# Kernel tuning notes

Measured on AMD Instinct MI355X. Metric: run time of the kernel, lower is better.

## Reference

```python
import jax, jax.numpy as jnp
import numpy as np

B, D, H, N, K, C = 1024, 256, 512, 100000, 96, 10


def setup_inputs() -> dict:
    key = jax.random.key(0)
    ks = jax.random.split(key, 16)
    s = 0.02
    return {
        "x": jax.random.normal(ks[0], (B, D), jnp.float32),
        "candidate_x": jax.random.normal(ks[1], (N, D), jnp.float32),
        "candidate_labels": jax.random.randint(ks[2], (N,), 0, C, jnp.int32),
        "W_enc": jax.random.normal(ks[3], (D, H), jnp.float32) * s,
        "b_enc": jnp.zeros((H,), jnp.float32),
        "W_key": jax.random.normal(ks[4], (H, H), jnp.float32) * s,
        "b_key": jnp.zeros((H,), jnp.float32),
        "W_val": jax.random.normal(ks[5], (H, H), jnp.float32) * s,
        "b_val": jnp.zeros((H,), jnp.float32),
        "E_label": jax.random.normal(ks[6], (C, H), jnp.float32) * s,
        "W_t1": jax.random.normal(ks[7], (H, H), jnp.float32) * s,
        "b_t1": jnp.zeros((H,), jnp.float32),
        "W_t2": jax.random.normal(ks[8], (H, H), jnp.float32) * s,
    }


def reference(x, candidate_x, candidate_labels, W_enc, b_enc, W_key, b_key,
              W_val, b_val, E_label, W_t1, b_t1, W_t2):
    # Encode queries and candidates
    x_enc = x @ W_enc + b_enc                       # [B, H]
    cand_enc = candidate_x @ W_enc + b_enc          # [N, H]
    x_key = x_enc @ W_key + b_key                   # [B, H]
    cand_keys = cand_enc @ W_key + b_key            # [N, H]

    # Negative euclidean distance via GEMM expansion (compute-efficient cdist)
    q2 = jnp.sum(x_key * x_key, axis=-1, keepdims=True)        # [B, 1]
    c2 = jnp.sum(cand_keys * cand_keys, axis=-1)               # [N]
    d2 = q2 + c2[None, :] - 2.0 * (x_key @ cand_keys.T)        # [B, N]
    sim = -jnp.sqrt(jnp.maximum(d2, 0.0))                      # [B, N]

    # Top-k retrieval
    top_sims, top_idx = jax.lax.top_k(sim, K)                  # [B, K]

    cand_vals = cand_enc @ W_val + b_val                       # [N, H]
    label_emb = E_label[candidate_labels]                      # [N, H]

    ctx_keys = cand_keys[top_idx]                              # [B, K, H]
    ctx_labels = label_emb[top_idx]                            # [B, K, H]
    _ = cand_vals[top_idx]  # gathered values (unused by the original math)

    # Attention over retrieved context (softmax of top-k similarities)
    attn = jax.nn.softmax(top_sims, axis=1)                    # [B, K]

    # Correction MLP T (dropout is identity in eval mode)
    diff = x_key[:, None, :] - ctx_keys                        # [B, K, H]
    t_out = jax.nn.relu(diff @ W_t1 + b_t1) @ W_t2             # [B, K, H]

    ctx_vec = jnp.sum(attn[..., None] * (ctx_labels + t_out), axis=1)  # [B, H]
    return x_enc + ctx_vec
```

## Files before the change

kernel.cpp:

```cpp
#include <hip/hip_runtime.h>
#include <cfloat>
#include <cmath>

#define B_ 1024
#define D_ 256
#define H_ 512
#define N_ 100000
#define K_ 96
#define C_ 10
#define SAMP 4096
#define CAPC 4096
#define RCAP 15

typedef __attribute__((ext_vector_type(8))) short bf16x8;
typedef __attribute__((ext_vector_type(4))) float f32x4;

__device__ __forceinline__ float bf2f(ushort h) {
    union { unsigned u; float f; } v; v.u = ((unsigned)h) << 16; return v.f;
}
__device__ __forceinline__ ushort f2bf(float f) {
    union { float f; unsigned u; } v; v.f = f;
    unsigned u = v.u;
    unsigned r = (u + 0x7fffu + ((u >> 16) & 1u)) >> 16;
    return (ushort)r;
}
__device__ __forceinline__ unsigned f2key(float f) {
    unsigned u = __float_as_uint(f);
    return (u & 0x80000000u) ? ~u : (u | 0x80000000u);
}
__device__ __forceinline__ float d2_of(float acc, float q2, float c2) {
    return fmaxf(fmaf(-2.f, acc, q2 + c2), 0.f);
}

#define GLDS(g, l)                                                            \
    __builtin_amdgcn_global_load_lds(                                         \
        (const __attribute__((address_space(1))) void*)(g),                   \
        (__attribute__((address_space(3))) void*)(l), 16, 0, 0)

#define FENCE() asm volatile("" ::: "memory")

template <int RELU>
__global__ __launch_bounds__(256) void gemm_nn(const float* __restrict__ A,
                                               const float* __restrict__ Bm,
                                               const float* __restrict__ bias,
                                               float* __restrict__ Cm,
                                               int M, int N, int Kd) {
    __shared__ float sA[16][68];
    __shared__ float sB[16][64];
    const int t  = threadIdx.x;
    const int tx = t & 15, ty = t >> 4;
    const int m0 = blockIdx.y * 64;
    const int n0 = blockIdx.x * 64;
    const int lr = t >> 2;
    const int lk = (t & 3) << 2;
    const int bk = t >> 4;
    const int bn = (t & 15) << 2;

    float acc[4][4] = {};
    for (int k0 = 0; k0 < Kd; k0 += 16) {
        float4 av = make_float4(0.f, 0.f, 0.f, 0.f);
        if (m0 + lr < M)
            av = *(const float4*)(A + (size_t)(m0 + lr) * Kd + k0 + lk);
        sA[lk + 0][lr] = av.x; sA[lk + 1][lr] = av.y;
        sA[lk + 2][lr] = av.z; sA[lk + 3][lr] = av.w;
        float4 bv = *(const float4*)(Bm + (size_t)(k0 + bk) * N + n0 + bn);
        *(float4*)&sB[bk][bn] = bv;
        __syncthreads();
#pragma unroll
        for (int kk = 0; kk < 16; ++kk) {
            float4 a4 = *(const float4*)&sA[kk][ty << 2];
            float4 b4 = *(const float4*)&sB[kk][tx << 2];
            float ar[4] = {a4.x, a4.y, a4.z, a4.w};
            float br[4] = {b4.x, b4.y, b4.z, b4.w};
#pragma unroll
            for (int i = 0; i < 4; ++i)
#pragma unroll
                for (int j = 0; j < 4; ++j)
                    acc[i][j] = fmaf(ar[i], br[j], acc[i][j]);
        }
        __syncthreads();
    }
#pragma unroll
    for (int i = 0; i < 4; ++i) {
        int row = m0 + (ty << 2) + i;
        if (row < M) {
            int col = n0 + (tx << 2);
            float b0 = 0.f, b1 = 0.f, b2 = 0.f, b3 = 0.f;
            if (bias) { b0 = bias[col]; b1 = bias[col + 1]; b2 = bias[col + 2]; b3 = bias[col + 3]; }
            float4 o;
            o.x = acc[i][0] + b0; o.y = acc[i][1] + b1;
            o.z = acc[i][2] + b2; o.w = acc[i][3] + b3;
            if (RELU) {
                o.x = fmaxf(o.x, 0.f); o.y = fmaxf(o.y, 0.f);
                o.z = fmaxf(o.z, 0.f); o.w = fmaxf(o.w, 0.f);
            }
            *(float4*)(Cm + (size_t)row * N + col) = o;
        }
    }
}

template <int MODE, int SWZ>
__global__ __launch_bounds__(256) void gemm_nt(const ushort* __restrict__ A,
                                               const ushort* __restrict__ Bv,
                                               const float* __restrict__ bias,
                                               const float* __restrict__ q2v,
                                               const float* __restrict__ c2v,
                                               const float* __restrict__ thrv,
                                               float* __restrict__ candV,
                                               int* __restrict__ candI,
                                               int* __restrict__ cnt,
                                               void* __restrict__ Cout,
                                               int M, int Nlim, int K,
                                               int ldc, int nvalid, int per) {
    int m0, n0;
    if (SWZ == 0) {
        m0 = blockIdx.y * 128; n0 = blockIdx.x * 128;
    } else if (SWZ == 1) {
        int bid = blockIdx.x;
        int xcd = bid & 7, slot = bid >> 3;
        m0 = (slot & 7) * 128;
        n0 = (xcd * per + (slot >> 3)) * 128;
        if (n0 >= nvalid || m0 >= M) return;
    } else {
        int bid = blockIdx.x;
        int xcd = bid & 7, slot = bid >> 3;
        n0 = (slot & 3) * 128;
        m0 = (xcd * per + (slot >> 2)) * 128;
        if (m0 >= M) return;
    }

    __shared__ __align__(16) char smem[32768];
    const int t = threadIdx.x;
    const int lane = t & 63, w = t >> 6;
    const int wm = w & 1, wn = w >> 1;

    f32x4 acc[4][4];
#pragma unroll
    for (int i = 0; i < 4; ++i)
#pragma unroll
        for (int j = 0; j < 4; ++j)
            acc[i][j] = (f32x4){0.f, 0.f, 0.f, 0.f};

    const int la = lane & 15, lk = lane >> 4;
    const int aoff = (wm * 64 + la) * 64 + lk * 16;
    const int boff = (wn * 64 + la) * 64 + lk * 16;
    const int r_ = t >> 2, cc_ = (t & 3);

    auto stage = [&](int k0, int buf) {
#pragma unroll
        for (int q = 0; q < 2; ++q) {
            int r = r_ + q * 64;
            int ar = m0 + r; ar = (ar < M) ? ar : (M - 1);
            GLDS(A + (size_t)ar * K + k0 + cc_ * 8,
                 (char*)smem + buf * 8192 + (q * 256 + t) * 16);
            int br = n0 + r; br = (br < Nlim) ? br : (Nlim - 1);
            GLDS(Bv + (size_t)br * K + k0 + cc_ * 8,
                 (char*)smem + 16384 + buf * 8192 + (q * 256 + t) * 16);
        }
    };

    stage(0, 0);
    int cur = 0;
    for (int k0 = 0; k0 < K; k0 += 32) {
        if (k0 + 32 < K) {
            stage(k0 + 32, cur ^ 1);
            FENCE();
            asm volatile("s_waitcnt vmcnt(4)" ::: "memory");
        } else {
            FENCE();
            asm volatile("s_waitcnt vmcnt(0)" ::: "memory");
        }
        __builtin_amdgcn_s_barrier(); FENCE();

        bf16x8 af[4], bfr[4];
        const char* pA = (const char*)smem + cur * 8192 + aoff;
        const char* pB = (const char*)smem + 16384 + cur * 8192 + boff;
#pragma unroll
        for (int i = 0; i < 4; ++i)
            af[i] = *(const bf16x8*)(pA + i * 1024);
#pragma unroll
        for (int j = 0; j < 4; ++j)
            bfr[j] = *(const bf16x8*)(pB + j * 1024);
#pragma unroll
        for (int i = 0; i < 4; ++i)
#pragma unroll
            for (int j = 0; j < 4; ++j)
                acc[i][j] = __builtin_amdgcn_mfma_f32_16x16x32_bf16(
                    af[i], bfr[j], acc[i][j], 0, 0, 0);

        FENCE();
        asm volatile("s_waitcnt lgkmcnt(0)" ::: "memory");
        __builtin_amdgcn_s_barrier(); FENCE();
        cur ^= 1;
    }

    const int rl = (lane >> 4) * 4, cl = lane & 15;

    if (MODE == 5) {
        float* stV = (float*)smem;
        int*   stI = (int*)(smem + 7680);
        int*   stC = (int*)(smem + 15360);
        for (int r = t; r < 128; r += 256) stC[r] = 0;
        __syncthreads();
#pragma unroll
        for (int i = 0; i < 4; ++i) {
#pragma unroll
            for (int v = 0; v < 4; ++v) {
                int rloc = wm * 64 + i * 16 + rl + v;
                int gr = m0 + rloc;
                float q2b = q2v[gr];
                float th = thrv[gr];
#pragma unroll
                for (int j = 0; j < 4; ++j) {
                    int gc = n0 + wn * 64 + j * 16 + cl;
                    if (gc < nvalid) {
                        float d2 = d2_of(acc[i][j][v], q2b, c2v[gc]);
                        if (d2 <= th) {
                            int p = atomicAdd(&stC[rloc], 1);
                            if (p < RCAP) {
                                stV[rloc * RCAP + p] = d2;
                                stI[rloc * RCAP + p] = gc;
                            } else {
                                int gp = atomicAdd(&cnt[gr], 1);
                                if (gp < CAPC) {
                                    candV[(size_t)gr * CAPC + gp] = d2;
                                    candI[(size_t)gr * CAPC + gp] = gc;
                                }
                            }
                        }
                    }
                }
            }
        }
        __syncthreads();
        for (int r = t; r < 128; r += 256) {
            int n = stC[r]; if (n > RCAP) n = RCAP;
            if (n > 0) {
                int gr = m0 + r;
                int gb = atomicAdd(&cnt[gr], n);
                for (int q = 0; q < n; ++q) {
                    int pos = gb + q;
                    if (pos < CAPC) {
                        candV[(size_t)gr * CAPC + pos] = stV[r * RCAP + q];
                        candI[(size_t)gr * CAPC + pos] = stI[r * RCAP + q];
                    }
                }
            }
        }
        return;
    }

#pragma unroll
    for (int i = 0; i < 4; ++i) {
#pragma unroll
        for (int j = 0; j < 4; ++j) {
            int gc = n0 + wn * 64 + j * 16 + cl;
#pragma unroll
            for (int v = 0; v < 4; ++v) {
                int gr = m0 + wm * 64 + i * 16 + rl + v;
                if (gr < M && gc < nvalid) {
                    float val = acc[i][j][v];
                    if (MODE == 2) {
                        ((float*)Cout)[(size_t)gr * ldc + gc] = val;
                    } else {
                        if (MODE == 1 || MODE == 3) val += bias[gc];
                        if (MODE == 1) val = fmaxf(val, 0.f);
                        ((ushort*)Cout)[(size_t)gr * ldc + gc] = f2bf(val);
                    }
                }
            }
        }
    }
}

__global__ __launch_bounds__(256) void thr_select(const float* __restrict__ S,
                                                  int ld,
                                                  const float* __restrict__ q2v,
                                                  const float* __restrict__ c2v,
                                                  float* __restrict__ thrArr) {
    __shared__ unsigned keys[SAMP];
    __shared__ int hist[256];
    __shared__ int sel[2];
    const int b = blockIdx.x, t = threadIdx.x;
    const float q2b = q2v[b];
    for (int i = t; i < SAMP; i += 256)
        keys[i] = ~f2key(d2_of(S[(size_t)b * ld + i], q2b, c2v[i]));
    __syncthreads();
    unsigned prefix = 0, mask = 0;
    int rank = K_;
    for (int shift = 24; shift >= 0; shift -= 8) {
        hist[t & 255] = 0;
        __syncthreads();
        for (int i = t; i < SAMP; i += 256) {
            unsigned k = keys[i];
            if ((k & mask) == prefix) atomicAdd(&hist[(k >> shift) & 255], 1);
        }
        __syncthreads();
        if (t == 0) {
            int r = rank, d = 255;
            for (; d > 0; --d) { int c = hist[d]; if (r - c <= 0) break; r -= c; }
            sel[0] = d; sel[1] = (r < 1) ? 1 : r;
        }
        __syncthreads();
        prefix |= ((unsigned)sel[0]) << shift;
        rank = sel[1];
        mask |= (0xFFu << shift);
        __syncthreads();
    }
    if (t == 0) {
        unsigned key = ~prefix;
        thrArr[b] = __uint_as_float(key & 0x7FFFFFFFu);
    }
}

__global__ __launch_bounds__(256) void final_select(const float* __restrict__ candV,
                                                    const int* __restrict__ candI,
                                                    const int* __restrict__ cnt,
                                                    float* __restrict__ topV,
                                                    int* __restrict__ topI) {
    __shared__ unsigned keys[CAPC];
    __shared__ int hist[256];
    __shared__ int sel[2];
    __shared__ int poscnt, eqcnt;
    const int b = blockIdx.x, t = threadIdx.x;
    int n = cnt[b]; if (n > CAPC) n = CAPC;
    for (int i = t; i < n; i += 256)
        keys[i] = ~f2key(candV[(size_t)b * CAPC + i]);
    __syncthreads();
    unsigned prefix = 0, mask = 0;
    int rank = K_;
    for (int shift = 24; shift >= 0; shift -= 8) {
        hist[t & 255] = 0;
        __syncthreads();
        for (int i = t; i < n; i += 256) {
            unsigned k = keys[i];
            if ((k & mask) == prefix) atomicAdd(&hist[(k >> shift) & 255], 1);
        }
        __syncthreads();
        if (t == 0) {
            int r = rank, d = 255;
            for (; d > 0; --d) { int c = hist[d]; if (r - c <= 0) break; r -= c; }
            sel[0] = d; sel[1] = (r < 1) ? 1 : r;
        }
        __syncthreads();
        prefix |= ((unsigned)sel[0]) << shift;
        rank = sel[1];
        mask |= (0xFFu << shift);
        __syncthreads();
    }
    unsigned kth = prefix;
    if (t == 0) { poscnt = 0; eqcnt = 0; }
    __syncthreads();
    for (int i = t; i < n; i += 256) {
        if (keys[i] > kth) {
            int p = atomicAdd(&poscnt, 1);
            topV[b * K_ + p] = candV[(size_t)b * CAPC + i];
            topI[b * K_ + p] = candI[(size_t)b * CAPC + i];
        }
    }
    __syncthreads();
    int base = poscnt;
    for (int i = t; i < n; i += 256) {
        if (keys[i] == kth) {
            int p = atomicAdd(&eqcnt, 1);
            if (base + p < K_) {
                topV[b * K_ + base + p] = candV[(size_t)b * CAPC + i];
                topI[b * K_ + base + p] = candI[(size_t)b * CAPC + i];
            }
        }
    }
}

__global__ void init_cnt(int* cnt) {
    int i = blockIdx.x * 256 + threadIdx.x;
    if (i < B_) cnt[i] = 0;
}

__global__ void conv_f2b(const float* __restrict__ in, ushort* __restrict__ out, int n) {
    int i = (blockIdx.x * 256 + threadIdx.x) * 4;
    int stride = gridDim.x * 256 * 4;
    for (; i < n; i += stride) {
        float4 v = *(const float4*)(in + i);
        ushort4 o;
        o.x = f2bf(v.x); o.y = f2bf(v.y); o.z = f2bf(v.z); o.w = f2bf(v.w);
        *(ushort4*)(out + i) = o;
    }
}

__global__ __launch_bounds__(256) void transpose_f2b(const float* __restrict__ in,
                                                     ushort* __restrict__ out,
                                                     int R, int Cn) {
    __shared__ float tile[32][33];
    int bx = blockIdx.x * 32, by = blockIdx.y * 32;
    int tx = threadIdx.x & 31, ty = threadIdx.x >> 5;
    int x = bx + tx;
#pragma unroll
    for (int dy = 0; dy < 32; dy += 8) {
        int y = by + ty + dy;
        if (x < Cn && y < R) tile[ty + dy][tx] = in[(size_t)y * Cn + x];
    }
    __syncthreads();
    int ox = by + tx;
#pragma unroll
    for (int dy = 0; dy < 32; dy += 8) {
        int oy = bx + ty + dy;
        if (ox < R && oy < Cn) out[(size_t)oy * R + ox] = f2bf(tile[tx][ty + dy]);
    }
}

__global__ __launch_bounds__(64) void rowsq_b(const ushort* __restrict__ X,
                                              float* __restrict__ outv) {
    const int r = blockIdx.x, t = threadIdx.x;
    const ushort* p = X + (size_t)r * H_;
    ushort4 a = *(const ushort4*)(p + t * 4);
    ushort4 b = *(const ushort4*)(p + 256 + t * 4);
    float ax = bf2f(a.x), ay = bf2f(a.y), az = bf2f(a.z), aw = bf2f(a.w);
    float bx = bf2f(b.x), by = bf2f(b.y), bz = bf2f(b.z), bw = bf2f(b.w);
    float v = ax * ax + ay * ay + az * az + aw * aw +
              bx * bx + by * by + bz * bz + bw * bw;
    for (int off = 32; off > 0; off >>= 1) v += __shfl_down(v, off);
    if (t == 0) outv[r] = v;
}

__global__ __launch_bounds__(64) void q2x_k(const ushort* __restrict__ Xb,
                                            const float* __restrict__ Xf,
                                            const float* __restrict__ bc,
                                            float* __restrict__ outv) {
    const int r = blockIdx.x, t = threadIdx.x;
    const ushort* p  = Xb + (size_t)r * H_ + t * 8;
    const float*  xf = Xf + (size_t)r * H_ + t * 8;
    float nrm = 0.f, dot = 0.f;
#pragma unroll
    for (int j = 0; j < 8; ++j) {
        float v = bf2f(p[j]);
        nrm = fmaf(v, v, nrm);
        dot = fmaf(xf[j], bc[t * 8 + j], dot);
    }
    for (int off = 32; off > 0; off >>= 1) {
        nrm += __shfl_down(nrm, off);
        dot += __shfl_down(dot, off);
    }
    if (t == 0) outv[r] = nrm - 2.f * dot;
}

__global__ void bcomb_k(const float* __restrict__ b_enc,
                        const float* __restrict__ W_key,
                        const float* __restrict__ b_key,
                        float* __restrict__ b_comb) {
    int h = blockIdx.x * 256 + threadIdx.x;
    if (h >= H_) return;
    float acc = b_key[h];
    for (int m = 0; m < H_; ++m)
        acc = fmaf(b_enc[m], W_key[(size_t)m * H_ + h], acc);
    b_comb[h] = acc;
}

__global__ __launch_bounds__(128) void softmax_k(const float* __restrict__ topVal,
                                                 float* __restrict__ attn) {
    __shared__ float red[128];
    const int b = blockIdx.x, t = threadIdx.x;
    float v = (t < K_) ? -sqrtf(topVal[b * K_ + t]) : -FLT_MAX;
    red[t] = v; __syncthreads();
    for (int s = 64; s > 0; s >>= 1) {
        if (t < s) red[t] = fmaxf(red[t], red[t + s]);
        __syncthreads();
    }
    float m = red[0]; __syncthreads();
    float e = (t < K_) ? expf(v - m) : 0.f;
    red[t] = e; __syncthreads();
    for (int s = 64; s > 0; s >>= 1) {
        if (t < s) red[t] += red[t + s];
        __syncthreads();
    }
    float ssum = red[0];
    if (t < K_) attn[b * K_ + t] = e / ssum;
}

__global__ __launch_bounds__(128) void gather_diff_b(const float* __restrict__ XK,
                                                     const ushort* __restrict__ CK,
                                                     const int* __restrict__ topI,
                                                     ushort* __restrict__ diff,
                                                     int b0) {
    const int r = blockIdx.x;
    const int b = b0 + r / K_;
    const int idx = topI[b * K_ + (r % K_)];
    const int t = threadIdx.x;
    float4 xv = *(const float4*)(XK + (size_t)b * H_ + t * 4);
    ushort4 cv = *(const ushort4*)(CK + (size_t)idx * H_ + t * 4);
    ushort4 o;
    o.x = f2bf(xv.x - bf2f(cv.x));
    o.y = f2bf(xv.y - bf2f(cv.y));
    o.z = f2bf(xv.z - bf2f(cv.z));
    o.w = f2bf(xv.w - bf2f(cv.w));
    *(ushort4*)(diff + (size_t)r * H_ + t * 4) = o;
}

__global__ __launch_bounds__(256) void wsum_h(const float* __restrict__ attn,
                                              const ushort* __restrict__ h,
                                              ushort* __restrict__ hw, int b0) {
    const int bl = blockIdx.x;
    const int b = b0 + bl;
    const int t = threadIdx.x;
    float a0 = 0.f, a1 = 0.f;
    const float* ap = attn + b * K_;
    for (int k = 0; k < K_; ++k) {
        float w = ap[k];
        const ushort* hr = h + (size_t)(bl * K_ + k) * H_;
        a0 = fmaf(w, bf2f(hr[t]), a0);
        a1 = fmaf(w, bf2f(hr[t + 256]), a1);
    }
    hw[(size_t)b * H_ + t]       = f2bf(a0);
    hw[(size_t)b * H_ + t + 256] = f2bf(a1);
}

__global__ __launch_bounds__(256) void final_out(const float* __restrict__ attn,
                                                 const int* __restrict__ topI,
                                                 const int* __restrict__ labels,
                                                 const float* __restrict__ E,
                                                 const float* __restrict__ tsum,
                                                 const float* __restrict__ xe,
                                                 float* __restrict__ out) {
    const int b = blockIdx.x, t = threadIdx.x;
    float a0 = 0.f, a1 = 0.f;
    for (int k = 0; k < K_; ++k) {
        float w = attn[b * K_ + k];
        int idx = topI[b * K_ + k];
        int lab = labels[idx];
        const float* el = E + (size_t)lab * H_;
        a0 = fmaf(w, el[t], a0);
        a1 = fmaf(w, el[t + 256], a1);
    }
    out[(size_t)b * H_ + t] =
        xe[(size_t)b * H_ + t] + a0 + tsum[(size_t)b * H_ + t];
    out[(size_t)b * H_ + t + 256] =
        xe[(size_t)b * H_ + t + 256] + a1 + tsum[(size_t)b * H_ + t + 256];
}

extern "C" void kernel_launch(void* const* d_in, const int* in_sizes, int n_in,
                              void* d_out, int out_size, void* d_ws, size_t ws_size,
                              hipStream_t stream) {
    const float* x      = (const float*)d_in[0];
    const float* cx     = (const float*)d_in[1];
    const int*   labels = (const int*)d_in[2];
    const float* W_enc  = (const float*)d_in[3];
    const float* b_enc  = (const float*)d_in[4];
    const float* W_key  = (const float*)d_in[5];
    const float* b_key  = (const float*)d_in[6];
    const float* E_label = (const float*)d_in[9];
    const float* W_t1   = (const float*)d_in[10];
    const float* b_t1   = (const float*)d_in[11];
    const float* W_t2   = (const float*)d_in[12];
    float* out = (float*)d_out;

    char* base = (char*)d_ws;
    size_t off = 0;
    auto take = [&](size_t n) -> char* {
        char* p = base + off;
        off = (off + n + 255) & ~(size_t)255;
        return p;
    };
    float*  Wc    = (float*)take((size_t)D_ * H_ * 4);
    float*  bc    = (float*)take((size_t)H_ * 4);
    ushort* WcT   = (ushort*)take((size_t)H_ * D_ * 2);
    ushort* Wcb   = (ushort*)take((size_t)D_ * H_ * 2);
    ushort* Wt1T  = (ushort*)take((size_t)H_ * H_ * 2);
    ushort* Wt2T  = (ushort*)take((size_t)H_ * H_ * 2);
    float*  xe    = (float*)take((size_t)B_ * H_ * 4);
    float*  xk    = (float*)take((size_t)B_ * H_ * 4);
    ushort* xkb   = (ushort*)take((size_t)B_ * H_ * 2);
    ushort* xprojb= (ushort*)take((size_t)B_ * D_ * 2);
    float*  q2x   = (float*)take((size_t)B_ * 4);
    ushort* ckb   = (ushort*)take((size_t)N_ * H_ * 2);
    float*  c2    = (float*)take((size_t)N_ * 4);
    float*  topV  = (float*)take((size_t)B_ * K_ * 4);
    int*    topI  = (int*)take((size_t)B_ * K_ * 4);
    float*  thr   = (float*)take((size_t)B_ * 4);
    float*  attn  = (float*)take((size_t)B_ * K_ * 4);
    int*    cnt   = (int*)take((size_t)B_ * 4);
    float*  candV = (float*)take((size_t)B_ * CAPC * 4);
    int*    candI = (int*)take((size_t)B_ * CAPC * 4);
    ushort* hwAll = (ushort*)take((size_t)B_ * H_ * 2);
    float*  tsum  = (float*)take((size_t)B_ * H_ * 4);
    char*   big   = base + off;
    size_t rem = (ws_size > off) ? (ws_size - off) : 0;

    ushort* cxb = (ushort*)big;
    float* simSmall = (float*)candV;

    long long bcq = (long long)(rem / ((size_t)K_ * H_ * 2 * 2));
    if (bcq > B_) bcq = B_;
    if (bcq < 1) bcq = 1;
    int Bc = (int)bcq;

    {
        dim3 g(H_ / 64, D_ / 64);
        gemm_nn<0><<<g, 256, 0, stream>>>(W_enc, W_key, nullptr, Wc, D_, H_, H_);
        bcomb_k<<<(H_ + 255) / 256, 256, 0, stream>>>(b_enc, W_key, b_key, bc);
        dim3 gt1((H_ + 31) / 32, (D_ + 31) / 32);
        transpose_f2b<<<gt1, 256, 0, stream>>>(Wc, WcT, D_, H_);
        conv_f2b<<<128, 256, 0, stream>>>(Wc, Wcb, D_ * H_);
        dim3 gt2((H_ + 31) / 32, (H_ + 31) / 32);
        transpose_f2b<<<gt2, 256, 0, stream>>>(W_t1, Wt1T, H_, H_);
        transpose_f2b<<<gt2, 256, 0, stream>>>(W_t2, Wt2T, H_, H_);
    }
    {
        dim3 gx(H_ / 64, B_ / 64);
        gemm_nn<0><<<gx, 256, 0, stream>>>(x, W_enc, b_enc, xe, B_, H_, D_);
        gemm_nn<0><<<gx, 256, 0, stream>>>(x, Wc, bc, xk, B_, H_, D_);
        conv_f2b<<<1024, 256, 0, stream>>>(xk, xkb, B_ * H_);
        conv_f2b<<<2048, 256, 0, stream>>>(cx, cxb, N_ * D_);
        dim3 gp(D_ / 128, B_ / 128);
        gemm_nt<0, 0><<<gp, 256, 0, stream>>>(
            xkb, Wcb, nullptr, nullptr, nullptr, nullptr, nullptr, nullptr,
            nullptr, xprojb, B_, D_, H_, D_, D_, 0);
        q2x_k<<<B_, 64, 0, stream>>>(xkb, xk, bc, q2x);
    }
    {
        int mt = (N_ + 127) / 128;
        int mper = (mt + 7) / 8;
        gemm_nt<3, 2><<<8 * mper * 4, 256, 0, stream>>>(
            cxb, WcT, bc, nullptr, nullptr, nullptr, nullptr, nullptr, nullptr,
            ckb, N_, H_, D_, H_, H_, mper);
    }
    rowsq_b<<<N_, 64, 0, stream>>>(ckb, c2);

    {
        int nper = (SAMP / 128 + 7) / 8;
        gemm_nt<2, 1><<<64 * nper, 256, 0, stream>>>(
            xprojb, cxb, nullptr, nullptr, nullptr, nullptr, nullptr, nullptr,
            nullptr, simSmall, B_, N_, D_, SAMP, SAMP, nper);
        thr_select<<<B_, 256, 0, stream>>>(simSmall, SAMP, q2x, c2, thr);
    }
    init_cnt<<<(B_ + 255) / 256, 256, 0, stream>>>(cnt);
    {
        int NT = (N_ + 127) / 128;
        int nper = (NT + 7) / 8;
        gemm_nt<5, 1><<<64 * nper, 256, 0, stream>>>(
            xprojb, cxb, nullptr, q2x, c2, thr, candV, candI, cnt,
            nullptr, B_, N_, D_, 0, N_, nper);
    }
    final_select<<<B_, 256, 0, stream>>>(candV, candI, cnt, topV, topI);
    softmax_k<<<B_, 128, 0, stream>>>(topV, attn);

    ushort* diffB = (ushort*)big;
    ushort* hB = (ushort*)(big + (size_t)Bc * K_ * H_ * 2);
    for (int b0 = 0; b0 < B_; b0 += Bc) {
        int bcn = min(Bc, B_ - b0);
        int Mrows = bcn * K_;
        gather_diff_b<<<Mrows, 128, 0, stream>>>(xk, ckb, topI, diffB, b0);
        int mt4 = (Mrows + 127) / 128;
        int mper4 = (mt4 + 7) / 8;
        gemm_nt<1, 2><<<8 * mper4 * 4, 256, 0, stream>>>(
            diffB, Wt1T, b_t1, nullptr, nullptr, nullptr, nullptr, nullptr,
            nullptr, hB, Mrows, H_, H_, H_, H_, mper4);
        wsum_h<<<bcn, 256, 0, stream>>>(attn, hB, hwAll, b0);
    }
    {
        dim3 g(H_ / 128, B_ / 128);
        gemm_nt<2, 0><<<g, 256, 0, stream>>>(
            hwAll, Wt2T, nullptr, nullptr, nullptr, nullptr, nullptr, nullptr,
            nullptr, tsum, B_, H_, H_, H_, H_, 0);
    }
    final_out<<<B_, 256, 0, stream>>>(attn, topI, labels, E_label, tsum, xe, out);
}
```

Before: 893.9 us.

## Split correction MLP first layer by linearity into per-query and per-candidate GEMMs

Rewrites relu((xk - ck)W1 + b1) as relu(P - Q), where P = xk·W1 + b1 is computed once per query and Q = ck·W1 once per candidate. The batched gather/diff/GEMM over B·K rows is replaced by a single N-row GEMM plus a fused gather, relu and attention-weighted sum kernel. This removes the materialized diff and hidden buffers and the chunk loop. It trades that for a gather of Q rows and a different rounding point, since Q is stored in bf16 before subtraction. The old path remains as a fallback when the workspace is too small.

```diff
diff --git a/kernel.cpp b/kernel.cpp
--- a/kernel.cpp
+++ b/kernel.cpp
@@ -262,6 +262,8 @@
                     float val = acc[i][j][v];
                     if (MODE == 2) {
                         ((float*)Cout)[(size_t)gr * ldc + gc] = val;
+                    } else if (MODE == 4) {
+                        ((float*)Cout)[(size_t)gr * ldc + gc] = val + bias[gc];
                     } else {
                         if (MODE == 1 || MODE == 3) val += bias[gc];
                         if (MODE == 1) val = fmaxf(val, 0.f);
@@ -474,6 +476,29 @@
     }
     float ssum = red[0];
     if (t < K_) attn[b * K_ + t] = e / ssum;
+}
+
+__global__ __launch_bounds__(256) void wsum_q(const float* __restrict__ attn,
+                                              const int* __restrict__ topI,
+                                              const float* __restrict__ P,
+                                              const ushort* __restrict__ Q,
+                                              ushort* __restrict__ hw) {
+    __shared__ float aw[K_];
+    __shared__ int ai[K_];
+    const int b = blockIdx.x, t = threadIdx.x;
+    if (t < K_) { aw[t] = attn[b * K_ + t]; ai[t] = topI[b * K_ + t]; }
+    __syncthreads();
+    const float p0 = P[(size_t)b * H_ + 2 * t];
+    const float p1 = P[(size_t)b * H_ + 2 * t + 1];
+    float a0 = 0.f, a1 = 0.f;
+    for (int k = 0; k < K_; ++k) {
+        float w = aw[k];
+        ushort2 q = *(const ushort2*)(Q + (size_t)ai[k] * H_ + 2 * t);
+        a0 = fmaf(w, fmaxf(p0 - bf2f(q.x), 0.f), a0);
+        a1 = fmaf(w, fmaxf(p1 - bf2f(q.y), 0.f), a1);
+    }
+    ushort2 o; o.x = f2bf(a0); o.y = f2bf(a1);
+    *(ushort2*)(hw + (size_t)b * H_ + 2 * t) = o;
 }
 
 __global__ __launch_bounds__(128) void gather_diff_b(const float* __restrict__ XK,
@@ -581,16 +606,12 @@
     int*    candI = (int*)take((size_t)B_ * CAPC * 4);
     ushort* hwAll = (ushort*)take((size_t)B_ * H_ * 2);
     float*  tsum  = (float*)take((size_t)B_ * H_ * 4);
+    float*  Pbuf  = (float*)take((size_t)B_ * H_ * 4);
     char*   big   = base + off;
     size_t rem = (ws_size > off) ? (ws_size - off) : 0;
 
     ushort* cxb = (ushort*)big;
     float* simSmall = (float*)candV;
-
-    long long bcq = (long long)(rem / ((size_t)K_ * H_ * 2 * 2));
-    if (bcq > B_) bcq = B_;
-    if (bcq < 1) bcq = 1;
-    int Bc = (int)bcq;
 
     {
         dim3 g(H_ / 64, D_ / 64);
@@ -614,6 +635,10 @@
             xkb, Wcb, nullptr, nullptr, nullptr, nullptr, nullptr, nullptr,
             nullptr, xprojb, B_, D_, H_, D_, D_, 0);
         q2x_k<<<B_, 64, 0, stream>>>(xkb, xk, bc, q2x);
+        dim3 gq(H_ / 128, B_ / 128);
+        gemm_nt<4, 0><<<gq, 256, 0, stream>>>(
+            xkb, Wt1T, b_t1, nullptr, nullptr, nullptr, nullptr, nullptr,
+            nullptr, Pbuf, B_, H_, H_, H_, H_, 0);
     }
     {
         int mt = (N_ + 127) / 128;
@@ -642,18 +667,32 @@
     final_select<<<B_, 256, 0, stream>>>(candV, candI, cnt, topV, topI);
     softmax_k<<<B_, 128, 0, stream>>>(topV, attn);
 
-    ushort* diffB = (ushort*)big;
-    ushort* hB = (ushort*)(big + (size_t)Bc * K_ * H_ * 2);
-    for (int b0 = 0; b0 < B_; b0 += Bc) {
-        int bcn = min(Bc, B_ - b0);
-        int Mrows = bcn * K_;
-        gather_diff_b<<<Mrows, 128, 0, stream>>>(xk, ckb, topI, diffB, b0);
-        int mt4 = (Mrows + 127) / 128;
-        int mper4 = (mt4 + 7) / 8;
-        gemm_nt<1, 2><<<8 * mper4 * 4, 256, 0, stream>>>(
-            diffB, Wt1T, b_t1, nullptr, nullptr, nullptr, nullptr, nullptr,
-            nullptr, hB, Mrows, H_, H_, H_, H_, mper4);
-        wsum_h<<<bcn, 256, 0, stream>>>(attn, hB, hwAll, b0);
+    if (rem >= (size_t)N_ * H_ * 2) {
+        ushort* Qb = (ushort*)big;
+        int mt = (N_ + 127) / 128;
+        int mper = (mt + 7) / 8;
+        gemm_nt<0, 2><<<8 * mper * 4, 256, 0, stream>>>(
+            ckb, Wt1T, nullptr, nullptr, nullptr, nullptr, nullptr, nullptr,
+            nullptr, Qb, N_, H_, H_, H_, H_, mper);
+        wsum_q<<<B_, 256, 0, stream>>>(attn, topI, Pbuf, Qb, hwAll);
+    } else {
+        long long bcq = (long long)(rem / ((size_t)K_ * H_ * 2 * 2));
+        if (bcq > B_) bcq = B_;
+        if (bcq < 1) bcq = 1;
+        int Bc = (int)bcq;
+        ushort* diffB = (ushort*)big;
+        ushort* hB = (ushort*)(big + (size_t)Bc * K_ * H_ * 2);
+        for (int b0 = 0; b0 < B_; b0 += Bc) {
+            int bcn = min(Bc, B_ - b0);
+            int Mrows = bcn * K_;
+            gather_diff_b<<<Mrows, 128, 0, stream>>>(xk, ckb, topI, diffB, b0);
+            int mt4 = (Mrows + 127) / 128;
+            int mper4 = (mt4 + 7) / 8;
+            gemm_nt<1, 2><<<8 * mper4 * 4, 256, 0, stream>>>(
+                diffB, Wt1T, b_t1, nullptr, nullptr, nullptr, nullptr, nullptr,
+                nullptr, hB, Mrows, H_, H_, H_, H_, mper4);
+            wsum_h<<<bcn, 256, 0, stream>>>(attn, hB, hwAll, b0);
+        }
     }
     {
         dim3 g(H_ / 128, B_ / 128);
```

After: 854.3 us. 1.05x faster.
